# Kernel optimization log

Hardware: AMD Instinct MI355X
Metric: run time of the kernel (lower is better)

Reference implementation:

```python
import jax, jax.numpy as jnp
import numpy as np

B, L1, CTX_TXT, C, NH, HD = 2, 4096, 512, 2048, 16, 128
IMG_LEN = 257           # hard-coded image-context length in WanI2VCrossAttentionProcessor
L2 = IMG_LEN + CTX_TXT
EPS = 1e-6


def setup_inputs() -> dict:
    key = jax.random.key(0)
    ks = jax.random.split(key, 16)
    s = 0.02
    w = lambda k: jax.random.normal(k, (C, C), jnp.float32) * s
    bvec = lambda k: jax.random.normal(k, (C,), jnp.float32) * s
    return {
        "x": jax.random.normal(ks[0], (B, L1, C), jnp.float32),
        "context": jax.random.normal(ks[1], (B, L2, C), jnp.float32),
        "context_lens": jax.random.randint(ks[2], (B,), 1, CTX_TXT + 1, jnp.int32),
        "Wq": w(ks[3]), "bq": bvec(ks[4]), "gq": jnp.ones((C,), jnp.float32),
        "Wk": w(ks[5]), "bk": bvec(ks[6]), "gk": jnp.ones((C,), jnp.float32),
        "Wv": w(ks[7]), "bv": bvec(ks[8]),
        "Wki": w(ks[9]), "bki": bvec(ks[10]), "gki": jnp.ones((C,), jnp.float32),
        "Wvi": w(ks[11]), "bvi": bvec(ks[12]),
        "Wo": w(ks[13]), "bo": bvec(ks[14]),
    }


def rms_norm(x, g):
    # RMSNorm over full channel dim (applied before head reshape, as in source)
    return x * jax.lax.rsqrt(jnp.mean(x * x, axis=-1, keepdims=True) + EPS) * g


def attention(q, k, v, key_mask=None):
    # q: [b, Lq, n, d]; k, v: [b, Lk, n, d]
    scale = 1.0 / np.sqrt(HD).astype(np.float32)
    scores = jnp.einsum('bqnd,bknd->bnqk', q, k) * scale
    if key_mask is not None:
        scores = jnp.where(key_mask, scores, jnp.finfo(scores.dtype).min)
    probs = jax.nn.softmax(scores, axis=-1)
    return jnp.einsum('bnqk,bknd->bqnd', probs, v)


def reference(x, context, context_lens, Wq, bq, gq, Wk, bk, gk, Wv, bv,
              Wki, bki, gki, Wvi, bvi, Wo, bo):
    b = x.shape[0]
    ctx_img = context[:, :IMG_LEN]
    ctx_txt = context[:, IMG_LEN:]

    q = rms_norm(x @ Wq + bq, gq).reshape(b, -1, NH, HD)
    k = rms_norm(ctx_txt @ Wk + bk, gk).reshape(b, -1, NH, HD)
    v = (ctx_txt @ Wv + bv).reshape(b, -1, NH, HD)
    k_img = rms_norm(ctx_img @ Wki + bki, gki).reshape(b, -1, NH, HD)
    v_img = (ctx_img @ Wvi + bvi).reshape(b, -1, NH, HD)

    img_x = attention(q, k_img, v_img)  # no k_lens on image branch
    key_mask = (jnp.arange(CTX_TXT)[None, :] < context_lens[:, None])[:, None, None, :]
    txt_x = attention(q, k, v, key_mask)

    out = (txt_x + img_x).reshape(b, -1, NH * HD)
    return out @ Wo + bo
```

## Files before the change

kernel.cpp:

```cpp
#include <hip/hip_runtime.h>

typedef unsigned short u16;
typedef short short8 __attribute__((ext_vector_type(8)));
typedef float f32x4 __attribute__((ext_vector_type(4)));
typedef unsigned short u16x4 __attribute__((ext_vector_type(4)));

__device__ __forceinline__ u16 f2bf(float f) {
  unsigned u = __builtin_bit_cast(unsigned, f);
  u += 0x7fffu + ((u >> 16) & 1u);
  return (u16)(u >> 16);
}
__device__ __forceinline__ float bf2f(u16 s) {
  unsigned u = ((unsigned)s) << 16;
  return __builtin_bit_cast(float, u);
}
__device__ __forceinline__ unsigned cvtpk_bf16(float a, float b) {
  unsigned r;
  asm("v_cvt_pk_bf16_f32 %0, %1, %2" : "=v"(r) : "v"(a), "v"(b));
  return r;
}

#if __has_builtin(__builtin_amdgcn_exp2f)
#define EXP2F(x) __builtin_amdgcn_exp2f(x)
#else
#define EXP2F(x) exp2f(x)
#endif

#define MFMA32(a, b, c) __builtin_amdgcn_mfma_f32_16x16x32_bf16(a, b, c, 0, 0, 0)

#define GLDS16(gp, lp)                                                         \
  __builtin_amdgcn_global_load_lds(                                            \
      (__attribute__((address_space(1))) void*)(gp),                           \
      (__attribute__((address_space(3))) void*)(lp), 16, 0, 0)

__global__ __launch_bounds__(256) void cast_bf16_k(const float* __restrict__ in,
                                                   u16* __restrict__ out, int n4) {
  int i = blockIdx.x * 256 + threadIdx.x;
  if (i >= n4) return;
  float4 v = ((const float4*)in)[i];
  u16x4 o = { f2bf(v.x), f2bf(v.y), f2bf(v.z), f2bf(v.w) };
  ((u16x4*)out)[i] = o;
}

__global__ __launch_bounds__(256) void transw_k(const float* W0, const float* W1,
                                                const float* W2, const float* W3,
                                                const float* W4, const float* W5,
                                                u16* __restrict__ Wt) {
  int z = blockIdx.z;
  const float* W = z == 0 ? W0 : z == 1 ? W1 : z == 2 ? W2 : z == 3 ? W3 : z == 4 ? W4 : W5;
  u16* T = Wt + (size_t)z * 2048 * 2048;
  __shared__ float tile[64][65];
  int k0 = blockIdx.x * 64, n0 = blockIdx.y * 64;
  int c4 = (threadIdx.x & 15) * 4;
  int r = threadIdx.x >> 4;
#pragma unroll
  for (int i = 0; i < 4; ++i) {
    int row = r + i * 16;
    float4 v = *(const float4*)(W + (size_t)(k0 + row) * 2048 + n0 + c4);
    tile[row][c4 + 0] = v.x; tile[row][c4 + 1] = v.y;
    tile[row][c4 + 2] = v.z; tile[row][c4 + 3] = v.w;
  }
  __syncthreads();
#pragma unroll
  for (int i = 0; i < 4; ++i) {
    int nrow = r + i * 16;
    u16x4 o = { f2bf(tile[c4 + 0][nrow]), f2bf(tile[c4 + 1][nrow]),
                f2bf(tile[c4 + 2][nrow]), f2bf(tile[c4 + 3][nrow]) };
    *(u16x4*)(T + (size_t)(n0 + nrow) * 2048 + k0 + c4) = o;
  }
}

struct GemmJob {
  const u16* A; const u16* Bt; const float* bias; void* out;
  int M; int mode; int ldo;
};
struct GemmJobs { GemmJob j[8]; };

__global__ __launch_bounds__(256) void gemm_k(GemmJobs jobs) {
  GemmJob J = jobs.j[blockIdx.z];
  const int m0 = blockIdx.x * 128;
  if (m0 >= J.M) return;
  const int n0 = blockIdx.y * 128;
  __shared__ u16 Asm[2][128 * 32];
  __shared__ u16 Bsm[2][128 * 32];
  const int tid = threadIdx.x;
  const int lane = tid & 63;
  const int l15 = lane & 15, quad = lane >> 4;
  const int wave = tid >> 6;
  const int wr = (wave >> 1) * 64, wc = (wave & 1) * 64;
  f32x4 acc[4][4] = {};
  const int g0 = tid, g1 = tid + 256;
  const u16* ag0 = J.A + (size_t)(m0 + (g0 >> 2)) * 2048 + (g0 & 3) * 8;
  const u16* ag1 = J.A + (size_t)(m0 + (g1 >> 2)) * 2048 + (g1 & 3) * 8;
  const u16* bg0 = J.Bt + (size_t)(n0 + (g0 >> 2)) * 2048 + (g0 & 3) * 8;
  const u16* bg1 = J.Bt + (size_t)(n0 + (g1 >> 2)) * 2048 + (g1 & 3) * 8;

  auto stage = [&](int buf, int k0) {
    GLDS16(ag0 + k0, &Asm[buf][g0 * 8]);
    GLDS16(ag1 + k0, &Asm[buf][g1 * 8]);
    GLDS16(bg0 + k0, &Bsm[buf][g0 * 8]);
    GLDS16(bg1 + k0, &Bsm[buf][g1 * 8]);
  };
  stage(0, 0);
  for (int k0 = 0; k0 < 2048; k0 += 32) {
    const int cb = (k0 >> 5) & 1;
    __syncthreads();
    if (k0 + 32 < 2048) stage(cb ^ 1, k0 + 32);
    short8 af[4], bf[4];
#pragma unroll
    for (int mi = 0; mi < 4; ++mi)
      af[mi] = *(const short8*)(&Asm[cb][(wr + mi * 16 + l15) * 32 + quad * 8]);
#pragma unroll
    for (int ni = 0; ni < 4; ++ni)
      bf[ni] = *(const short8*)(&Bsm[cb][(wc + ni * 16 + l15) * 32 + quad * 8]);
    __builtin_amdgcn_s_setprio(1);
#pragma unroll
    for (int mi = 0; mi < 4; ++mi)
#pragma unroll
      for (int ni = 0; ni < 4; ++ni)
        acc[mi][ni] = __builtin_amdgcn_mfma_f32_16x16x32_bf16(af[mi], bf[ni], acc[mi][ni], 0, 0, 0);
    __builtin_amdgcn_s_setprio(0);
  }
#pragma unroll
  for (int mi = 0; mi < 4; ++mi) {
#pragma unroll
    for (int ni = 0; ni < 4; ++ni) {
      int nn = n0 + wc + ni * 16 + l15;
      float bv = J.bias[nn];
#pragma unroll
      for (int r = 0; r < 4; ++r) {
        int mm = m0 + wr + mi * 16 + quad * 4 + r;
        if (mm >= J.M) continue;
        float v = acc[mi][ni][r] + bv;
        if (J.mode == 0) {
          ((u16*)J.out)[(size_t)mm * J.ldo + nn] = f2bf(v);
        } else if (J.mode == 1) {
          int ml = mm & 31;
          int mp = (mm & ~31) | (((ml >> 2) & 3) * 8 + (ml >> 4) * 4 + (ml & 3));
          ((u16*)J.out)[(size_t)nn * J.ldo + mp] = f2bf(v);
        } else {
          ((float*)J.out)[(size_t)mm * J.ldo + nn] = v;
        }
      }
    }
  }
}

__global__ __launch_bounds__(512, 2) void gemm256_k(const u16* __restrict__ A,
                                                    const u16* __restrict__ Bt,
                                                    const float* __restrict__ bias,
                                                    void* __restrict__ out,
                                                    int mode) {
  const int m0 = blockIdx.x * 256, n0 = blockIdx.y * 256;
  __shared__ u16 lds[2][2][256 * 64];
  const int tid = threadIdx.x, lane = tid & 63;
  const int l15 = lane & 15, quad = lane >> 4;
  const int wave = tid >> 6;
  const int wr = wave >> 2;
  const int wc = wave & 3;
  f32x4 acc[8][4] = {};

  auto stage = [&](int buf, int kt) {
    const int ko = kt * 64;
#pragma unroll
    for (int j = 0; j < 4; ++j) {
      const int c = tid + 512 * j;
      const int row = c >> 3;
      const int scc = (((c & 7) ^ (row & 7)) * 8);
      GLDS16(A + (size_t)(m0 + row) * 2048 + ko + scc, &lds[buf][0][(size_t)c * 8]);
      GLDS16(Bt + (size_t)(n0 + row) * 2048 + ko + scc, &lds[buf][1][(size_t)c * 8]);
    }
  };

  stage(0, 0);
  for (int t = 0; t < 32; ++t) {
    const int cb = t & 1;
    __syncthreads();
    if (t + 1 < 32) stage(cb ^ 1, t + 1);
    const u16* Ab = &lds[cb][0][0];
    const u16* Bb = &lds[cb][1][0];
    short8 bfr[2][4];
#pragma unroll
    for (int kk = 0; kk < 2; ++kk)
#pragma unroll
      for (int ni = 0; ni < 4; ++ni) {
        const int rn = wc * 64 + ni * 16 + l15;
        bfr[kk][ni] = *(const short8*)(Bb + rn * 64 + (((kk * 4 + quad) ^ (rn & 7)) * 8));
      }
#pragma unroll
    for (int mi = 0; mi < 8; ++mi) {
      const int rm = wr * 128 + mi * 16 + l15;
      short8 a0 = *(const short8*)(Ab + rm * 64 + (((0 + quad) ^ (rm & 7)) * 8));
      short8 a1 = *(const short8*)(Ab + rm * 64 + (((4 + quad) ^ (rm & 7)) * 8));
      __builtin_amdgcn_s_setprio(1);
#pragma unroll
      for (int ni = 0; ni < 4; ++ni)
        acc[mi][ni] = MFMA32(a0, bfr[0][ni], acc[mi][ni]);
#pragma unroll
      for (int ni = 0; ni < 4; ++ni)
        acc[mi][ni] = MFMA32(a1, bfr[1][ni], acc[mi][ni]);
      __builtin_amdgcn_s_setprio(0);
    }
  }
#pragma unroll
  for (int mi = 0; mi < 8; ++mi) {
#pragma unroll
    for (int ni = 0; ni < 4; ++ni) {
      const int nn = n0 + wc * 64 + ni * 16 + l15;
      const float bv = bias[nn];
      const int mm = m0 + wr * 128 + mi * 16 + quad * 4;
      if (mode == 0) {
        u16* op = (u16*)out + (size_t)mm * 2048 + nn;
#pragma unroll
        for (int r = 0; r < 4; ++r) op[(size_t)r * 2048] = f2bf(acc[mi][ni][r] + bv);
      } else {
        float* op = (float*)out + (size_t)mm * 2048 + nn;
#pragma unroll
        for (int r = 0; r < 4; ++r) op[(size_t)r * 2048] = acc[mi][ni][r] + bv;
      }
    }
  }
}

__global__ __launch_bounds__(256) void rmsnorm_k(u16* __restrict__ buf,
                                                 const float* __restrict__ g) {
  const int row = blockIdx.x, tid = threadIdx.x;
  u16* p = buf + (size_t)row * 2048 + tid * 8;
  short8 v = *(short8*)p;
  float x[8]; float s = 0.f;
#pragma unroll
  for (int i = 0; i < 8; ++i) { x[i] = bf2f((u16)v[i]); s += x[i] * x[i]; }
#pragma unroll
  for (int o = 1; o < 64; o <<= 1) s += __shfl_xor(s, o, 64);
  __shared__ float ws4[4];
  if ((tid & 63) == 0) ws4[tid >> 6] = s;
  __syncthreads();
  float tot = ws4[0] + ws4[1] + ws4[2] + ws4[3];
  float scale = rsqrtf(tot * (1.0f / 2048.0f) + 1e-6f);
  const float* gp = g + tid * 8;
  short8 o8;
#pragma unroll
  for (int i = 0; i < 8; ++i) o8[i] = (short)f2bf(x[i] * scale * gp[i]);
  *(short8*)p = o8;
}

__global__ __launch_bounds__(512) void attn_k(const u16* __restrict__ Q,
                                              const u16* __restrict__ Kt,
                                              const u16* __restrict__ Vt,
                                              const u16* __restrict__ Ki,
                                              const u16* __restrict__ Vi,
                                              const int* __restrict__ lens,
                                              u16* __restrict__ out) {
  const int lid = blockIdx.x + 16 * (blockIdx.y + 16 * blockIdx.z);
  const int xcd = lid & 7, i = lid >> 3;
  const int h = xcd * 2 + (i & 1);
  const int b = (i >> 1) & 1;
  const int qx = i >> 2;

  const int tid = threadIdx.x, lane = tid & 63, wave = tid >> 6;
  const int l15 = lane & 15, quad = lane >> 4;
  const int qbase = qx * 256 + wave * 32;
  const float scale2 = 0.12752358514837517f;
  const float NEGINF = -__builtin_inff();
  __shared__ u16 Ksm[2][2][32 * 128];
  __shared__ u16 Vsm[2][2][128 * 32];

  short8 qf[2][4];
#pragma unroll
  for (int h2 = 0; h2 < 2; ++h2) {
    const u16* qb = Q + ((size_t)(b * 4096 + qbase + h2 * 16 + l15)) * 2048 + h * 128 + quad * 8;
#pragma unroll
    for (int kc = 0; kc < 4; ++kc) qf[h2][kc] = *(const short8*)(qb + kc * 32);
  }

  const int krow = tid >> 4;
  const int kcc = ((tid & 15) ^ (krow & 7)) * 8;
  const int vd = tid >> 2;
  const int vcs = ((tid & 3) ^ ((vd >> 1) & 3)) * 8;
  const int kxor = l15 & 7;
  const int vxor = (l15 >> 1) & 3;

  f32x4 accv[2][8];
  u16x4 oimg[2][8];
  float run_m[2], run_l[2];

  auto phase = [&](const u16* Kb, const u16* Vb, int Lv, int LK) {
    run_m[0] = run_m[1] = NEGINF;
    run_l[0] = run_l[1] = 0.f;
#pragma unroll
    for (int h2 = 0; h2 < 2; ++h2)
#pragma unroll
      for (int dt = 0; dt < 8; ++dt)
#pragma unroll
        for (int r = 0; r < 4; ++r) accv[h2][dt][r] = 0.f;
    const u16* kg = Kb + (size_t)krow * 2048 + kcc;
    const u16* vg = Vb + (size_t)vd * LK + vcs;
    const int ntiles = (Lv + 63) >> 6;
    auto stage = [&](int buf, int t) {
      const int kvA = t * 64;
      const int sA = (kvA < LK - 32) ? kvA : (LK - 32);
      const int sB = (kvA + 32 < LK - 32) ? (kvA + 32) : (LK - 32);
      GLDS16(kg + (size_t)sA * 2048, &Ksm[buf][0][tid * 8]);
      GLDS16(kg + (size_t)sB * 2048, &Ksm[buf][1][tid * 8]);
      GLDS16(vg + sA, &Vsm[buf][0][tid * 8]);
      GLDS16(vg + sB, &Vsm[buf][1][tid * 8]);
    };
    stage(0, 0);
    __syncthreads();
    for (int t = 0; t < ntiles; ++t) {
      const int cb = t & 1;
      if (t + 1 < ntiles) stage(cb ^ 1, t + 1);

      f32x4 s[2][4];
#pragma unroll
      for (int h2 = 0; h2 < 2; ++h2)
#pragma unroll
        for (int kb = 0; kb < 4; ++kb)
#pragma unroll
          for (int r = 0; r < 4; ++r) s[h2][kb][r] = 0.f;
      {
        short8 kA[2][4];
#pragma unroll
        for (int kc = 0; kc < 4; ++kc) {
          const int c0 = ((kc * 4 + quad) ^ kxor) * 8;
          kA[0][kc] = *(const short8*)(&Ksm[cb][0][l15 * 128 + c0]);
          kA[1][kc] = *(const short8*)(&Ksm[cb][0][(16 + l15) * 128 + c0]);
        }
        __builtin_amdgcn_s_setprio(1);
#pragma unroll
        for (int h2 = 0; h2 < 2; ++h2)
#pragma unroll
          for (int kc = 0; kc < 4; ++kc) {
            s[h2][0] = MFMA32(kA[0][kc], qf[h2][kc], s[h2][0]);
            s[h2][1] = MFMA32(kA[1][kc], qf[h2][kc], s[h2][1]);
          }
        __builtin_amdgcn_s_setprio(0);
      }
      {
        short8 kB[2][4];
#pragma unroll
        for (int kc = 0; kc < 4; ++kc) {
          const int c0 = ((kc * 4 + quad) ^ kxor) * 8;
          kB[0][kc] = *(const short8*)(&Ksm[cb][1][l15 * 128 + c0]);
          kB[1][kc] = *(const short8*)(&Ksm[cb][1][(16 + l15) * 128 + c0]);
        }
        __builtin_amdgcn_s_setprio(1);
#pragma unroll
        for (int h2 = 0; h2 < 2; ++h2)
#pragma unroll
          for (int kc = 0; kc < 4; ++kc) {
            s[h2][2] = MFMA32(kB[0][kc], qf[h2][kc], s[h2][2]);
            s[h2][3] = MFMA32(kB[1][kc], qf[h2][kc], s[h2][3]);
          }
        __builtin_amdgcn_s_setprio(0);
      }

      const int kvA = t * 64;
      if (kvA + 64 > Lv) {
#pragma unroll
        for (int h2 = 0; h2 < 2; ++h2)
#pragma unroll
          for (int kb = 0; kb < 4; ++kb)
#pragma unroll
            for (int r = 0; r < 4; ++r) {
              const int ki = kvA + kb * 16 + quad * 4 + r;
              if (ki >= Lv) s[h2][kb][r] = NEGINF;
            }
      }

      float al[2];
      short8 pfA[2], pfB[2];
#pragma unroll
      for (int h2 = 0; h2 < 2; ++h2) {
        float m0 = fmaxf(fmaxf(s[h2][0][0], s[h2][0][1]), fmaxf(s[h2][0][2], s[h2][0][3]));
        float m1 = fmaxf(fmaxf(s[h2][1][0], s[h2][1][1]), fmaxf(s[h2][1][2], s[h2][1][3]));
        float m2 = fmaxf(fmaxf(s[h2][2][0], s[h2][2][1]), fmaxf(s[h2][2][2], s[h2][2][3]));
        float m3 = fmaxf(fmaxf(s[h2][3][0], s[h2][3][1]), fmaxf(s[h2][3][2], s[h2][3][3]));
        float mx = fmaxf(fmaxf(m0, m1), fmaxf(m2, m3));
        mx = fmaxf(mx, __shfl_xor(mx, 16, 64));
        mx = fmaxf(mx, __shfl_xor(mx, 32, 64));
        const float nm = (mx - run_m[h2] > 62.0f) ? mx : run_m[h2];
        al[h2] = EXP2F((run_m[h2] - nm) * scale2);
        run_m[h2] = nm;
        const float nmc = -nm * scale2;
        float p[4][4], psum = 0.f;
#pragma unroll
        for (int kb = 0; kb < 4; ++kb)
#pragma unroll
          for (int r = 0; r < 4; ++r) {
            p[kb][r] = EXP2F(__builtin_fmaf(s[h2][kb][r], scale2, nmc));
            psum += p[kb][r];
          }
        run_l[h2] = __builtin_fmaf(run_l[h2], al[h2], psum);
        union { short8 s8; unsigned u[4]; } pa, pb;
        pa.u[0] = cvtpk_bf16(p[0][0], p[0][1]);
        pa.u[1] = cvtpk_bf16(p[0][2], p[0][3]);
        pa.u[2] = cvtpk_bf16(p[1][0], p[1][1]);
        pa.u[3] = cvtpk_bf16(p[1][2], p[1][3]);
        pb.u[0] = cvtpk_bf16(p[2][0], p[2][1]);
        pb.u[1] = cvtpk_bf16(p[2][2], p[2][3]);
        pb.u[2] = cvtpk_bf16(p[3][0], p[3][1]);
        pb.u[3] = cvtpk_bf16(p[3][2], p[3][3]);
        pfA[h2] = pa.s8;
        pfB[h2] = pb.s8;
      }
      if (t != 0 && __ballot((al[0] < 1.0f) || (al[1] < 1.0f))) {
#pragma unroll
        for (int h2 = 0; h2 < 2; ++h2)
#pragma unroll
          for (int dt = 0; dt < 8; ++dt)
#pragma unroll
            for (int r = 0; r < 4; ++r) accv[h2][dt][r] *= al[h2];
      }

      __builtin_amdgcn_s_setprio(1);
#pragma unroll
      for (int dt = 0; dt < 8; ++dt) {
        const int vo = (dt * 16 + l15) * 32 + ((quad ^ vxor) * 8);
        short8 vfA = *(const short8*)(&Vsm[cb][0][vo]);
        short8 vfB = *(const short8*)(&Vsm[cb][1][vo]);
        accv[0][dt] = MFMA32(vfA, pfA[0], accv[0][dt]);
        accv[1][dt] = MFMA32(vfA, pfA[1], accv[1][dt]);
        accv[0][dt] = MFMA32(vfB, pfB[0], accv[0][dt]);
        accv[1][dt] = MFMA32(vfB, pfB[1], accv[1][dt]);
      }
      __builtin_amdgcn_s_setprio(0);
      __syncthreads();
    }
  };

  const u16* Kb_i = Ki + (size_t)(b * 288) * 2048 + h * 128;
  const u16* Vb_i = Vi + ((size_t)(b * 16 + h) * 128) * 288;
  phase(Kb_i, Vb_i, 257, 288);
#pragma unroll
  for (int h2 = 0; h2 < 2; ++h2) {
    float a = run_l[h2] + __shfl_xor(run_l[h2], 16, 64);
    float lt = a + __shfl_xor(a, 32, 64);
    float inv = 1.0f / lt;
#pragma unroll
    for (int dt = 0; dt < 8; ++dt) {
      u16x4 w2 = { f2bf(accv[h2][dt][0] * inv), f2bf(accv[h2][dt][1] * inv),
                   f2bf(accv[h2][dt][2] * inv), f2bf(accv[h2][dt][3] * inv) };
      oimg[h2][dt] = w2;
    }
  }
  const u16* Kb_t = Kt + (size_t)(b * 512) * 2048 + h * 128;
  const u16* Vb_t = Vt + ((size_t)(b * 16 + h) * 128) * 512;
  phase(Kb_t, Vb_t, lens[b], 512);
#pragma unroll
  for (int h2 = 0; h2 < 2; ++h2) {
    float a = run_l[h2] + __shfl_xor(run_l[h2], 16, 64);
    float lt = a + __shfl_xor(a, 32, 64);
    float inv = 1.0f / lt;
    u16* ob = out + ((size_t)(b * 4096 + qbase + h2 * 16 + l15)) * 2048 + h * 128 + quad * 4;
#pragma unroll
    for (int dt = 0; dt < 8; ++dt) {
      u16x4 w2 = { f2bf(bf2f(oimg[h2][dt][0]) + accv[h2][dt][0] * inv),
                   f2bf(bf2f(oimg[h2][dt][1]) + accv[h2][dt][1] * inv),
                   f2bf(bf2f(oimg[h2][dt][2]) + accv[h2][dt][2] * inv),
                   f2bf(bf2f(oimg[h2][dt][3]) + accv[h2][dt][3] * inv) };
      *(u16x4*)(ob + dt * 16) = w2;
    }
  }
}

extern "C" void kernel_launch(void* const* d_in, const int* in_sizes, int n_in,
                              void* d_out, int out_size, void* d_ws, size_t ws_size,
                              hipStream_t stream) {
  const float* x   = (const float*)d_in[0];
  const float* ctx = (const float*)d_in[1];
  const int* lens  = (const int*)d_in[2];
  const float* Wq  = (const float*)d_in[3];
  const float* bq  = (const float*)d_in[4];
  const float* gq  = (const float*)d_in[5];
  const float* Wk  = (const float*)d_in[6];
  const float* bk  = (const float*)d_in[7];
  const float* gk  = (const float*)d_in[8];
  const float* Wv  = (const float*)d_in[9];
  const float* bv  = (const float*)d_in[10];
  const float* Wki = (const float*)d_in[11];
  const float* bki = (const float*)d_in[12];
  const float* gki = (const float*)d_in[13];
  const float* Wvi = (const float*)d_in[14];
  const float* bvi = (const float*)d_in[15];
  const float* Wo  = (const float*)d_in[16];
  const float* bo  = (const float*)d_in[17];
  float* out = (float*)d_out;

  char* p = (char*)d_ws;
  u16* x_bf   = (u16*)p; p += (size_t)8192 * 2048 * 2;
  u16* ctx_bf = (u16*)p; p += (size_t)2 * 769 * 2048 * 2;
  u16* Wt     = (u16*)p; p += (size_t)6 * 2048 * 2048 * 2;
  u16* Qb     = (u16*)p; p += (size_t)8192 * 2048 * 2;
  u16* Ktxt   = (u16*)p; p += (size_t)2 * 512 * 2048 * 2;
  u16* Vtt    = (u16*)p; p += (size_t)2 * 16 * 128 * 512 * 2;
  u16* Kimg   = (u16*)p; p += (size_t)2 * 288 * 2048 * 2;
  u16* Vti    = (u16*)p; p += (size_t)2 * 16 * 128 * 288 * 2;
  u16* attn_o = x_bf;

  cast_bf16_k<<<16384, 256, 0, stream>>>(x, x_bf, 8192 * 2048 / 4);
  cast_bf16_k<<<3076, 256, 0, stream>>>(ctx, ctx_bf, 2 * 769 * 2048 / 4);
  transw_k<<<dim3(32, 32, 6), 256, 0, stream>>>(Wq, Wk, Wv, Wki, Wvi, Wo, Wt);

  gemm256_k<<<dim3(32, 8), 512, 0, stream>>>(x_bf, Wt + 0ull * 4194304, bq, Qb, 0);

  GemmJobs jc = {};
  for (int b = 0; b < 2; ++b) {
    const u16* txtA = ctx_bf + (size_t)(b * 769 + 257) * 2048;
    const u16* imgA = ctx_bf + (size_t)(b * 769) * 2048;
    jc.j[0 + b] = { txtA, Wt + 1ull * 4194304, bk,  Ktxt + (size_t)b * 512 * 2048, 512, 0, 2048 };
    jc.j[2 + b] = { txtA, Wt + 2ull * 4194304, bv,  Vtt  + (size_t)b * 2048 * 512, 512, 1, 512 };
    jc.j[4 + b] = { imgA, Wt + 3ull * 4194304, bki, Kimg + (size_t)b * 288 * 2048, 257, 0, 2048 };
    jc.j[6 + b] = { imgA, Wt + 4ull * 4194304, bvi, Vti  + (size_t)b * 2048 * 288, 257, 1, 288 };
  }
  gemm_k<<<dim3(4, 16, 8), 256, 0, stream>>>(jc);

  rmsnorm_k<<<8192, 256, 0, stream>>>(Qb, gq);
  rmsnorm_k<<<1024, 256, 0, stream>>>(Ktxt, gk);
  rmsnorm_k<<<576, 256, 0, stream>>>(Kimg, gki);

  attn_k<<<dim3(16, 16, 2), 512, 0, stream>>>(Qb, Ktxt, Vtt, Kimg, Vti, lens, attn_o);

  gemm256_k<<<dim3(32, 8), 512, 0, stream>>>(attn_o, Wt + 5ull * 4194304, bo, out, 1);
}
```

Before: 502.9 us.

## Pipeline 256-tile GEMM by half-tiles and loop batches inside attention blocks

The 256x256 GEMM is restructured to stage A/B operands in 128-row halves across a deeper pipeline. Loads for future k-tiles are interleaved with MFMA quarter-steps using explicit vmcnt waits, barriers and sched_barriers, aiming to hide global-load latency better. Separately, the attention kernel now launches half the blocks and loops over both batches inside each block, reducing grid size so each block does two batches' work. The attention change lowers parallelism to 256 blocks, which may underfill the GPU, and the many extra barriers in the GEMM add sync cost.

```diff
diff --git a/kernel.cpp b/kernel.cpp
--- a/kernel.cpp
+++ b/kernel.cpp
@@ -152,7 +152,7 @@
                                                     void* __restrict__ out,
                                                     int mode) {
   const int m0 = blockIdx.x * 256, n0 = blockIdx.y * 256;
-  __shared__ u16 lds[2][2][256 * 64];
+  __shared__ u16 lds[2][2][2][128 * 64];
   const int tid = threadIdx.x, lane = tid & 63;
   const int l15 = lane & 15, quad = lane >> 4;
   const int wave = tid >> 6;
@@ -160,46 +160,74 @@
   const int wc = wave & 3;
   f32x4 acc[8][4] = {};
 
-  auto stage = [&](int buf, int kt) {
-    const int ko = kt * 64;
-#pragma unroll
-    for (int j = 0; j < 4; ++j) {
-      const int c = tid + 512 * j;
+  auto stageH = [&](int op, int half, int kt) {
+    const int buf = kt & 1;
+    const u16* base = (op == 0 ? A + (size_t)(m0 + half * 128) * 2048
+                               : Bt + (size_t)(n0 + half * 128) * 2048) + kt * 64;
+#pragma unroll
+    for (int jj = 0; jj < 2; ++jj) {
+      const int c = tid + 512 * jj;
       const int row = c >> 3;
-      const int scc = (((c & 7) ^ (row & 7)) * 8);
-      GLDS16(A + (size_t)(m0 + row) * 2048 + ko + scc, &lds[buf][0][(size_t)c * 8]);
-      GLDS16(Bt + (size_t)(n0 + row) * 2048 + ko + scc, &lds[buf][1][(size_t)c * 8]);
+      const int scc = ((c & 7) ^ (row & 7)) * 8;
+      GLDS16(base + (size_t)row * 2048 + scc, &lds[buf][op][half][(size_t)c * 8]);
     }
   };
 
-  stage(0, 0);
-  for (int t = 0; t < 32; ++t) {
-    const int cb = t & 1;
-    __syncthreads();
-    if (t + 1 < 32) stage(cb ^ 1, t + 1);
-    const u16* Ab = &lds[cb][0][0];
-    const u16* Bb = &lds[cb][1][0];
-    short8 bfr[2][4];
-#pragma unroll
-    for (int kk = 0; kk < 2; ++kk)
-#pragma unroll
-      for (int ni = 0; ni < 4; ++ni) {
-        const int rn = wc * 64 + ni * 16 + l15;
-        bfr[kk][ni] = *(const short8*)(Bb + rn * 64 + (((kk * 4 + quad) ^ (rn & 7)) * 8));
-      }
-#pragma unroll
-    for (int mi = 0; mi < 8; ++mi) {
-      const int rm = wr * 128 + mi * 16 + l15;
-      short8 a0 = *(const short8*)(Ab + rm * 64 + (((0 + quad) ^ (rm & 7)) * 8));
-      short8 a1 = *(const short8*)(Ab + rm * 64 + (((4 + quad) ^ (rm & 7)) * 8));
-      __builtin_amdgcn_s_setprio(1);
-#pragma unroll
-      for (int ni = 0; ni < 4; ++ni)
-        acc[mi][ni] = MFMA32(a0, bfr[0][ni], acc[mi][ni]);
-#pragma unroll
-      for (int ni = 0; ni < 4; ++ni)
-        acc[mi][ni] = MFMA32(a1, bfr[1][ni], acc[mi][ni]);
-      __builtin_amdgcn_s_setprio(0);
+  stageH(0, 0, 0); stageH(0, 1, 0); stageH(1, 0, 0); stageH(1, 1, 0);
+  stageH(0, 0, 1); stageH(0, 1, 1); stageH(1, 0, 1); stageH(1, 1, 1);
+  asm volatile("s_waitcnt vmcnt(8)" ::: "memory");
+  __builtin_amdgcn_s_barrier();
+
+  for (int i = 0; i < 16; ++i) {
+#pragma unroll
+    for (int hi = 0; hi < 2; ++hi) {
+      const int buf = hi;
+      short8 bfr[2][4], af[2][2];
+#pragma unroll
+      for (int q = 0; q < 4; ++q) {
+        if (q == 0) {
+#pragma unroll
+          for (int kc = 0; kc < 2; ++kc)
+#pragma unroll
+            for (int ni = 0; ni < 4; ++ni) {
+              const int r = (wc * 64 + ni * 16 + l15) & 127;
+              bfr[kc][ni] = *(const short8*)(
+                  &lds[buf][1][wc >> 1][r * 64 + (((kc * 4 + quad) ^ (r & 7)) * 8)]);
+            }
+        }
+#pragma unroll
+        for (int kc = 0; kc < 2; ++kc)
+#pragma unroll
+          for (int m2 = 0; m2 < 2; ++m2) {
+            const int r = (q * 2 + m2) * 16 + l15;
+            af[kc][m2] = *(const short8*)(
+                &lds[buf][0][wr][r * 64 + (((kc * 4 + quad) ^ (r & 7)) * 8)]);
+          }
+        {
+          const int p = hi * 4 + q;
+          const int op = (p == 2 || p == 3 || p == 6 || p == 7) ? 1 : 0;
+          const int hf = p & 1;
+          const int kt = (p < 2) ? (2 * i + 1) : ((p < 6) ? (2 * i + 2) : (2 * i + 3));
+          if (kt < 32 && !(i == 0 && p < 2)) stageH(op, hf, kt);
+        }
+        if (q == 3) {
+          if (i < 15) asm volatile("s_waitcnt vmcnt(4)" ::: "memory");
+          else        asm volatile("s_waitcnt vmcnt(0)" ::: "memory");
+        }
+        __builtin_amdgcn_s_barrier();
+        asm volatile("s_waitcnt lgkmcnt(0)" ::: "memory");
+        __builtin_amdgcn_sched_barrier(0);
+        __builtin_amdgcn_s_setprio(1);
+#pragma unroll
+        for (int m2 = 0; m2 < 2; ++m2)
+#pragma unroll
+          for (int ni = 0; ni < 4; ++ni) {
+            acc[q * 2 + m2][ni] = MFMA32(af[0][m2], bfr[0][ni], acc[q * 2 + m2][ni]);
+            acc[q * 2 + m2][ni] = MFMA32(af[1][m2], bfr[1][ni], acc[q * 2 + m2][ni]);
+          }
+        __builtin_amdgcn_s_setprio(0);
+        __builtin_amdgcn_s_barrier();
+      }
     }
   }
 #pragma unroll
@@ -251,11 +279,10 @@
                                               const u16* __restrict__ Vi,
                                               const int* __restrict__ lens,
                                               u16* __restrict__ out) {
-  const int lid = blockIdx.x + 16 * (blockIdx.y + 16 * blockIdx.z);
-  const int xcd = lid & 7, i = lid >> 3;
-  const int h = xcd * 2 + (i & 1);
-  const int b = (i >> 1) & 1;
-  const int qx = i >> 2;
+  const int lid = blockIdx.x + 16 * blockIdx.y;
+  const int xcd = lid & 7, j = lid >> 3;
+  const int h = xcd * 2 + (j & 1);
+  const int qx = j >> 1;
 
   const int tid = threadIdx.x, lane = tid & 63, wave = tid >> 6;
   const int l15 = lane & 15, quad = lane >> 4;
@@ -265,14 +292,6 @@
   __shared__ u16 Ksm[2][2][32 * 128];
   __shared__ u16 Vsm[2][2][128 * 32];
 
-  short8 qf[2][4];
-#pragma unroll
-  for (int h2 = 0; h2 < 2; ++h2) {
-    const u16* qb = Q + ((size_t)(b * 4096 + qbase + h2 * 16 + l15)) * 2048 + h * 128 + quad * 8;
-#pragma unroll
-    for (int kc = 0; kc < 4; ++kc) qf[h2][kc] = *(const short8*)(qb + kc * 32);
-  }
-
   const int krow = tid >> 4;
   const int kcc = ((tid & 15) ^ (krow & 7)) * 8;
   const int vd = tid >> 2;
@@ -280,6 +299,7 @@
   const int kxor = l15 & 7;
   const int vxor = (l15 >> 1) & 3;
 
+  short8 qf[2][4];
   f32x4 accv[2][8];
   u16x4 oimg[2][8];
   float run_m[2], run_l[2];
@@ -429,37 +449,45 @@
     }
   };
 
-  const u16* Kb_i = Ki + (size_t)(b * 288) * 2048 + h * 128;
-  const u16* Vb_i = Vi + ((size_t)(b * 16 + h) * 128) * 288;
-  phase(Kb_i, Vb_i, 257, 288);
-#pragma unroll
-  for (int h2 = 0; h2 < 2; ++h2) {
-    float a = run_l[h2] + __shfl_xor(run_l[h2], 16, 64);
-    float lt = a + __shfl_xor(a, 32, 64);
-    float inv = 1.0f / lt;
-#pragma unroll
-    for (int dt = 0; dt < 8; ++dt) {
-      u16x4 w2 = { f2bf(accv[h2][dt][0] * inv), f2bf(accv[h2][dt][1] * inv),
-                   f2bf(accv[h2][dt][2] * inv), f2bf(accv[h2][dt][3] * inv) };
-      oimg[h2][dt] = w2;
-    }
-  }
-  const u16* Kb_t = Kt + (size_t)(b * 512) * 2048 + h * 128;
-  const u16* Vb_t = Vt + ((size_t)(b * 16 + h) * 128) * 512;
-  phase(Kb_t, Vb_t, lens[b], 512);
-#pragma unroll
-  for (int h2 = 0; h2 < 2; ++h2) {
-    float a = run_l[h2] + __shfl_xor(run_l[h2], 16, 64);
-    float lt = a + __shfl_xor(a, 32, 64);
-    float inv = 1.0f / lt;
-    u16* ob = out + ((size_t)(b * 4096 + qbase + h2 * 16 + l15)) * 2048 + h * 128 + quad * 4;
-#pragma unroll
-    for (int dt = 0; dt < 8; ++dt) {
-      u16x4 w2 = { f2bf(bf2f(oimg[h2][dt][0]) + accv[h2][dt][0] * inv),
-                   f2bf(bf2f(oimg[h2][dt][1]) + accv[h2][dt][1] * inv),
-                   f2bf(bf2f(oimg[h2][dt][2]) + accv[h2][dt][2] * inv),
-                   f2bf(bf2f(oimg[h2][dt][3]) + accv[h2][dt][3] * inv) };
-      *(u16x4*)(ob + dt * 16) = w2;
+  for (int b = 0; b < 2; ++b) {
+#pragma unroll
+    for (int h2 = 0; h2 < 2; ++h2) {
+      const u16* qb = Q + ((size_t)(b * 4096 + qbase + h2 * 16 + l15)) * 2048 + h * 128 + quad * 8;
+#pragma unroll
+      for (int kc = 0; kc < 4; ++kc) qf[h2][kc] = *(const short8*)(qb + kc * 32);
+    }
+    const u16* Kb_i = Ki + (size_t)(b * 288) * 2048 + h * 128;
+    const u16* Vb_i = Vi + ((size_t)(b * 16 + h) * 128) * 288;
+    phase(Kb_i, Vb_i, 257, 288);
+#pragma unroll
+    for (int h2 = 0; h2 < 2; ++h2) {
+      float a = run_l[h2] + __shfl_xor(run_l[h2], 16, 64);
+      float lt = a + __shfl_xor(a, 32, 64);
+      float inv = 1.0f / lt;
+#pragma unroll
+      for (int dt = 0; dt < 8; ++dt) {
+        u16x4 w2 = { f2bf(accv[h2][dt][0] * inv), f2bf(accv[h2][dt][1] * inv),
+                     f2bf(accv[h2][dt][2] * inv), f2bf(accv[h2][dt][3] * inv) };
+        oimg[h2][dt] = w2;
+      }
+    }
+    const u16* Kb_t = Kt + (size_t)(b * 512) * 2048 + h * 128;
+    const u16* Vb_t = Vt + ((size_t)(b * 16 + h) * 128) * 512;
+    phase(Kb_t, Vb_t, lens[b], 512);
+#pragma unroll
+    for (int h2 = 0; h2 < 2; ++h2) {
+      float a = run_l[h2] + __shfl_xor(run_l[h2], 16, 64);
+      float lt = a + __shfl_xor(a, 32, 64);
+      float inv = 1.0f / lt;
+      u16* ob = out + ((size_t)(b * 4096 + qbase + h2 * 16 + l15)) * 2048 + h * 128 + quad * 4;
+#pragma unroll
+      for (int dt = 0; dt < 8; ++dt) {
+        u16x4 w2 = { f2bf(bf2f(oimg[h2][dt][0]) + accv[h2][dt][0] * inv),
+                     f2bf(bf2f(oimg[h2][dt][1]) + accv[h2][dt][1] * inv),
+                     f2bf(bf2f(oimg[h2][dt][2]) + accv[h2][dt][2] * inv),
+                     f2bf(bf2f(oimg[h2][dt][3]) + accv[h2][dt][3] * inv) };
+        *(u16x4*)(ob + dt * 16) = w2;
+      }
     }
   }
 }
@@ -519,7 +547,7 @@
   rmsnorm_k<<<1024, 256, 0, stream>>>(Ktxt, gk);
   rmsnorm_k<<<576, 256, 0, stream>>>(Kimg, gki);
 
-  attn_k<<<dim3(16, 16, 2), 512, 0, stream>>>(Qb, Ktxt, Vtt, Kimg, Vti, lens, attn_o);
+  attn_k<<<dim3(16, 16, 1), 512, 0, stream>>>(Qb, Ktxt, Vtt, Kimg, Vti, lens, attn_o);
 
   gemm256_k<<<dim3(32, 8), 512, 0, stream>>>(attn_o, Wt + 5ull * 4194304, bo, out, 1);
 }
```

Result: no change. 503.7 us (+0.2%).
